# Kernel tuning notes

Measured on AMD Instinct MI355X. Metric: run time of the kernel, lower is better.

Reference implementation:

```python
import jax, jax.numpy as jnp
import numpy as np

N_NODES = 50000
N_EDGES = 800000
IN_F, HID, NCLS = 128, 64, 64
N_EXTRA = 2          # layer - 2
K_STEPS = 10
ALPHA = 0.1
BN_EPS = 1e-5


def setup_inputs() -> dict:
    key = jax.random.key(0)
    ks = jax.random.split(key, 20)
    d = {}
    d['x'] = jax.random.normal(ks[0], (N_NODES, IN_F), dtype=jnp.float32)
    d['edge_index'] = jax.random.randint(ks[1], (2, N_EDGES), 0, N_NODES, dtype=jnp.int64)
    s = 1.0 / np.sqrt(HID)
    d['W1'] = jax.random.normal(ks[2], (IN_F, HID), dtype=jnp.float32) / np.sqrt(IN_F)
    d['b1'] = jnp.zeros((HID,), jnp.float32)
    d['W2'] = jax.random.normal(ks[3], (HID, HID), dtype=jnp.float32) * s
    d['b2'] = jnp.zeros((HID,), jnp.float32)
    d['Wx'] = jax.random.normal(ks[4], (N_EXTRA, HID, HID), dtype=jnp.float32) * s
    d['bx'] = jnp.zeros((N_EXTRA, HID), jnp.float32)
    d['g1'] = jnp.ones((HID,), jnp.float32); d['be1'] = jnp.zeros((HID,), jnp.float32)
    d['g2'] = jnp.ones((HID,), jnp.float32); d['be2'] = jnp.zeros((HID,), jnp.float32)
    d['g3'] = jnp.ones((HID,), jnp.float32); d['be3'] = jnp.zeros((HID,), jnp.float32)
    d['Wfc'] = jax.random.normal(ks[5], (HID, NCLS), dtype=jnp.float32) * s
    d['bfc'] = jnp.zeros((NCLS,), jnp.float32)
    return d


def _gcn_norm(edge_index, n):
    # add self-loops, symmetric D^-1/2 (A+I) D^-1/2 normalization (PyG GCNConv default)
    loop = jnp.arange(n, dtype=edge_index.dtype)
    src = jnp.concatenate([edge_index[0], loop])
    dst = jnp.concatenate([edge_index[1], loop])
    deg = jax.ops.segment_sum(jnp.ones(src.shape[0], jnp.float32), dst, num_segments=n)
    dinv = jnp.where(deg > 0, jax.lax.rsqrt(deg), 0.0)
    return src, dst, dinv[src] * dinv[dst]


def _propagate(x, src, dst, w, n):
    # gather-scale-scatter: out[dst] += w * x[src]
    return jax.ops.segment_sum(x[src] * w[:, None], dst, num_segments=n)


def _bn(x, g, b):
    # BatchNorm1d in training mode: batch statistics over the node dim
    m = jnp.mean(x, axis=0)
    v = jnp.var(x, axis=0)
    return g * (x - m) * jax.lax.rsqrt(v + BN_EPS) + b


def reference(x, edge_index, W1, b1, W2, b2, Wx, bx, g1, be1, g2, be2, g3, be3, Wfc, bfc):
    n = x.shape[0]
    src, dst, w = _gcn_norm(edge_index, n)
    h = _propagate(x @ W1, src, dst, w, n) + b1
    h = jax.nn.relu(_bn(h, g1, be1))
    h = _propagate(h @ W2, src, dst, w, n) + b2
    h = jax.nn.relu(_bn(h, g2, be2))
    for i in range(Wx.shape[0]):
        h = _propagate(h @ Wx[i], src, dst, w, n) + bx[i]
        h = jax.nn.relu(_bn(h, g3, be3))
    # APPNP: K power-iteration steps with teleport back to h0
    h0 = h
    for _ in range(K_STEPS):
        h = (1.0 - ALPHA) * _propagate(h, src, dst, w, n) + ALPHA * h0
    out = h @ Wfc + bfc
    return jax.nn.log_softmax(out, axis=1)
```

## Files before the change

kernel.cpp:

```cpp
#include <hip/hip_runtime.h>
#include <hip/hip_fp16.h>
#include <cstdint>
#include <cstddef>

#define NN 50000
#define NE 800000
#define HID 64
#define INF_ 128
#define BN_EPS 1e-5f
#define NGRP (NN / 8)
#define NG16 (NN / 16)
#define SCAN_B 196
#define NSLICE 32
#define NBKT 16
#define NBIN 196
#define EPB 2048
#define BCAP 5120

typedef float floatx2 __attribute__((ext_vector_type(2)));

__device__ __forceinline__ float4 h8_to_f4(float2 raw) {
    union { float f; __half2 h; } ua, ub;
    ua.f = raw.x; ub.f = raw.y;
    float2 fa = __half22float2(ua.h), fb = __half22float2(ub.h);
    return make_float4(fa.x, fa.y, fb.x, fb.y);
}
__device__ __forceinline__ float2 f4_to_h8(float4 v) {
    union { float f; __half2 h; } ua, ub;
    ua.h = __float22half2_rn(make_float2(v.x, v.y));
    ub.h = __float22half2_rn(make_float2(v.z, v.w));
    return make_float2(ua.f, ub.f);
}
struct f8 { float v[8]; };
__device__ __forceinline__ f8 h16_to_f8(float4 raw) {
    f8 r;
    union { float f; __half2 h; } u;
    float2 a;
    u.f = raw.x; a = __half22float2(u.h); r.v[0] = a.x; r.v[1] = a.y;
    u.f = raw.y; a = __half22float2(u.h); r.v[2] = a.x; r.v[3] = a.y;
    u.f = raw.z; a = __half22float2(u.h); r.v[4] = a.x; r.v[5] = a.y;
    u.f = raw.w; a = __half22float2(u.h); r.v[6] = a.x; r.v[7] = a.y;
    return r;
}
__device__ __forceinline__ float4 f8_to_h16(const f8& s) {
    union { float f; __half2 h; } u;
    float4 o;
    u.h = __float22half2_rn(make_float2(s.v[0], s.v[1])); o.x = u.f;
    u.h = __float22half2_rn(make_float2(s.v[2], s.v[3])); o.y = u.f;
    u.h = __float22half2_rn(make_float2(s.v[4], s.v[5])); o.z = u.f;
    u.h = __float22half2_rn(make_float2(s.v[6], s.v[7])); o.w = u.f;
    return o;
}

__device__ __forceinline__ void fp8x8_to_f(unsigned lo, unsigned hi, float out[8]) {
    floatx2 a = __builtin_amdgcn_cvt_pk_f32_fp8((int)lo, false);
    floatx2 b = __builtin_amdgcn_cvt_pk_f32_fp8((int)lo, true);
    floatx2 c = __builtin_amdgcn_cvt_pk_f32_fp8((int)hi, false);
    floatx2 d = __builtin_amdgcn_cvt_pk_f32_fp8((int)hi, true);
    out[0] = a[0]; out[1] = a[1]; out[2] = b[0]; out[3] = b[1];
    out[4] = c[0]; out[5] = c[1]; out[6] = d[0]; out[7] = d[1];
}
__device__ __forceinline__ void fp8x16_to_f(uint4 r, float out[16]) {
    fp8x8_to_f(r.x, r.y, out);
    fp8x8_to_f(r.z, r.w, out + 8);
}
__device__ __forceinline__ uint2 f_to_fp8x8(const float v[8]) {
    int w0 = __builtin_amdgcn_cvt_pk_fp8_f32(v[0], v[1], 0, false);
    w0 = __builtin_amdgcn_cvt_pk_fp8_f32(v[2], v[3], w0, true);
    int w1 = __builtin_amdgcn_cvt_pk_fp8_f32(v[4], v[5], 0, false);
    w1 = __builtin_amdgcn_cvt_pk_fp8_f32(v[6], v[7], w1, true);
    uint2 o; o.x = (unsigned)w0; o.y = (unsigned)w1;
    return o;
}
__device__ __forceinline__ uint4 f_to_fp8x16(const float v[16]) {
    uint2 a = f_to_fp8x8(v), b = f_to_fp8x8(v + 8);
    uint4 o; o.x = a.x; o.y = a.y; o.z = b.x; o.w = b.y;
    return o;
}


__global__ __launch_bounds__(256) void binscat_k(
        const int* __restrict__ src, const int* __restrict__ dst,
        int* __restrict__ bcur, int2* __restrict__ pairs) {
    __shared__ int lcnt[256], lscan[256], lexc[256], gbase[256];
    __shared__ int2 stage[EPB];
    const int t = threadIdx.x;
    const int base = blockIdx.x * EPB;
    lcnt[t] = 0;
    __syncthreads();
    int2 mypair[EPB / 256];
    int mybin[EPB / 256], myr[EPB / 256];
#pragma unroll
    for (int i = 0; i < EPB / 256; ++i) {
        int e = base + i * 256 + t;
        if (e < NE) {
            int s = src[e], d = dst[e];
            mypair[i] = make_int2(s, d);
            mybin[i] = d >> 8;
            myr[i] = atomicAdd(&lcnt[mybin[i]], 1);
        } else mybin[i] = -1;
    }
    __syncthreads();
    lscan[t] = lcnt[t];
    __syncthreads();
    for (int d = 1; d < 256; d <<= 1) {
        int u = (t >= d) ? lscan[t - d] : 0;
        __syncthreads();
        lscan[t] += u;
        __syncthreads();
    }
    lexc[t] = lscan[t] - lcnt[t];
    if (lcnt[t] > 0) gbase[t] = atomicAdd(&bcur[t], lcnt[t]);
    __syncthreads();
#pragma unroll
    for (int i = 0; i < EPB / 256; ++i)
        if (mybin[i] >= 0) stage[lexc[mybin[i]] + myr[i]] = mypair[i];
    __syncthreads();
    const int total = lscan[255];
#pragma unroll
    for (int i = 0; i < EPB / 256; ++i) {
        int s = i * 256 + t;
        if (s < total) {
            int2 pr = stage[s];
            int b = pr.y >> 8;
            pairs[(size_t)b * BCAP + gbase[b] + (s - lexc[b])] = pr;
        }
    }
}

__global__ __launch_bounds__(256) void bincnt_k(
        const int2* __restrict__ pairs, const int* __restrict__ bcur,
        int* __restrict__ deg, float* __restrict__ dinv, int* __restrict__ hist) {
    __shared__ int lc[256];
    __shared__ int lh[NBKT];
    const int b = blockIdx.x, t = threadIdx.x;
    lc[t] = 0;
    if (t < NBKT) lh[t] = 0;
    __syncthreads();
    const int cnt = bcur[b];
    const size_t s0 = (size_t)b * BCAP;
    for (int s = t; s < cnt; s += 256)
        atomicAdd(&lc[pairs[s0 + s].y & 255], 1);
    __syncthreads();
    int n = b * 256 + t;
    if (n < NN) {
        int d = lc[t];
        deg[n] = d;
        dinv[n] = rsqrtf((float)(d + 1));
        int c = (d + 7) >> 3;
        if (c > NBKT - 1) c = NBKT - 1;
        atomicAdd(&lh[c], 1);
    }
    __syncthreads();
    if (t < NBKT && lh[t]) atomicAdd(&hist[t], lh[t]);
}

__global__ __launch_bounds__(256) void scan1perm_k(
        const int* __restrict__ deg, const int* __restrict__ hist,
        int* __restrict__ offs, int* __restrict__ bsum,
        int* __restrict__ bktcur, int* __restrict__ perm) {
    __shared__ int sh[256];
    __shared__ int lh[NBKT], lbase[NBKT];
    const int t = threadIdx.x, b = blockIdx.x;
    const int i = b * 256 + t;
    const int dg = (i < NN) ? deg[i] : 0;
    if (t < NBKT) lh[t] = 0;
    __syncthreads();
    int c = 0, r = 0;
    if (i < NN) {
        c = (dg + 7) >> 3;
        if (c > NBKT - 1) c = NBKT - 1;
        r = atomicAdd(&lh[c], 1);
    }
    __syncthreads();
    if (t < NBKT) {
        int s = 0;
        for (int k = 0; k < t; ++k) s += hist[k];
        lbase[t] = s + (lh[t] ? atomicAdd(&bktcur[t], lh[t]) : 0);
    }
    __syncthreads();
    if (i < NN) perm[lbase[c] + r] = i;
    int v = (i < NN) ? ((dg + 7) & ~7) : 0;
    sh[t] = v;
    __syncthreads();
    for (int d = 1; d < 256; d <<= 1) {
        int u = (t >= d) ? sh[t - d] : 0;
        __syncthreads();
        sh[t] += u;
        __syncthreads();
    }
    if (i < NN) offs[i] = sh[t] - v;
    if (t == 255) bsum[b] = sh[255];
}

__global__ __launch_bounds__(256) void scan23_k(
        const int* __restrict__ bsum, int* __restrict__ offs) {
    __shared__ int sh[256];
    const int t = threadIdx.x, b = blockIdx.x;
    int v = (t < SCAN_B) ? bsum[t] : 0;
    sh[t] = v;
    __syncthreads();
    for (int d = 1; d < 256; d <<= 1) {
        int u = (t >= d) ? sh[t - d] : 0;
        __syncthreads();
        sh[t] += u;
        __syncthreads();
    }
    const int bpre = (b > 0) ? sh[b - 1] : 0;
    const int total = sh[SCAN_B - 1];
    const int i = b * 256 + t;
    if (i < NN) offs[i] += bpre;
    if (i == NN) offs[NN] = total;
}

__global__ __launch_bounds__(256) void binplace_pad_k(
        const int* __restrict__ bcur, const int2* __restrict__ pairs,
        const int* __restrict__ offs, int* __restrict__ edge1,
        float4* __restrict__ tmpH, uint4* __restrict__ x8a,
        uint4* __restrict__ x8b) {
    __shared__ int lcur[256];
    const int b = blockIdx.x, t = threadIdx.x;
    if (b == 0) {
        if (t < 8) tmpH[(size_t)NN * 8 + t] = make_float4(0.f, 0.f, 0.f, 0.f);
        else if (t < 12) x8a[(size_t)NN * 4 + (t - 8)] = make_uint4(0, 0, 0, 0);
        else if (t < 16) x8b[(size_t)NN * 4 + (t - 12)] = make_uint4(0, 0, 0, 0);
    }
    lcur[t] = 0;
    __syncthreads();
    const int cnt = bcur[b];
    const size_t s0 = (size_t)b * BCAP;
    for (int s = t; s < cnt; s += 256) {
        int2 pr = pairs[s0 + s];
        int d = pr.y;
        int slot = atomicAdd(&lcur[d & 255], 1);
        edge1[offs[d] + slot] = pr.x;
    }
    __syncthreads();
    int n = b * 256 + t;
    if (n < NN) {
        int e = offs[n] + lcur[t], e1 = offs[n + 1];
        for (; e < e1; ++e) edge1[e] = NN;
    }
}

template <int K, bool HIN>
__global__ __launch_bounds__(256, 2) void mm_k(const void* __restrict__ Xv,
                                               const float* __restrict__ W,
                                               const float* __restrict__ dinv,
                                               float2* __restrict__ Y) {
    constexpr int RS = K + 4;
    __shared__ float Xs[64 * RS];
    __shared__ float Ws[K * 64];
    const int t = threadIdx.x;
    const int n0 = blockIdx.x * 64;

    {
        const float4* Wg = (const float4*)W;
        for (int g2 = t; g2 < K * 16; g2 += 256) {
            int row = g2 >> 4, c4 = g2 & 15;
            *(float4*)&Ws[row * 64 + c4 * 4] = Wg[g2];
        }
    }
    if (HIN) {
        const float4* Xg = (const float4*)Xv;
        for (int g2 = t; g2 < 64 * (K / 8); g2 += 256) {
            int row = g2 / (K / 8), c8 = g2 % (K / 8);
            int rr = n0 + row; if (rr >= NN) rr = NN - 1;
            f8 v = h16_to_f8(Xg[(size_t)rr * (K / 8) + c8]);
            float* dp = &Xs[row * RS + c8 * 8];
#pragma unroll
            for (int j = 0; j < 8; ++j) dp[j] = v.v[j];
        }
    } else {
        const float4* Xg = (const float4*)Xv;
        for (int g2 = t; g2 < 64 * (K / 4); g2 += 256) {
            int row = g2 / (K / 4), c4 = g2 % (K / 4);
            int rr = n0 + row; if (rr >= NN) rr = NN - 1;
            *(float4*)&Xs[row * RS + c4 * 4] = Xg[(size_t)rr * (K / 4) + c4];
        }
    }
    __syncthreads();

    const int r0 = (t >> 4) << 2;
    const int c0 = (t & 15) << 2;
    float acc[4][4];
#pragma unroll
    for (int j = 0; j < 4; ++j)
#pragma unroll
        for (int c = 0; c < 4; ++c) acc[j][c] = 0.f;

#pragma unroll 8
    for (int kq = 0; kq < K / 4; ++kq) {
        float4 xv[4];
#pragma unroll
        for (int j = 0; j < 4; ++j)
            xv[j] = *(const float4*)&Xs[(r0 + j) * RS + kq * 4];
        float4 wv[4];
#pragma unroll
        for (int i = 0; i < 4; ++i)
            wv[i] = *(const float4*)&Ws[(kq * 4 + i) * 64 + c0];
#pragma unroll
        for (int j = 0; j < 4; ++j) {
            acc[j][0] = fmaf(xv[j].x, wv[0].x, acc[j][0]);
            acc[j][1] = fmaf(xv[j].x, wv[0].y, acc[j][1]);
            acc[j][2] = fmaf(xv[j].x, wv[0].z, acc[j][2]);
            acc[j][3] = fmaf(xv[j].x, wv[0].w, acc[j][3]);
            acc[j][0] = fmaf(xv[j].y, wv[1].x, acc[j][0]);
            acc[j][1] = fmaf(xv[j].y, wv[1].y, acc[j][1]);
            acc[j][2] = fmaf(xv[j].y, wv[1].z, acc[j][2]);
            acc[j][3] = fmaf(xv[j].y, wv[1].w, acc[j][3]);
            acc[j][0] = fmaf(xv[j].z, wv[2].x, acc[j][0]);
            acc[j][1] = fmaf(xv[j].z, wv[2].y, acc[j][1]);
            acc[j][2] = fmaf(xv[j].z, wv[2].z, acc[j][2]);
            acc[j][3] = fmaf(xv[j].z, wv[2].w, acc[j][3]);
            acc[j][0] = fmaf(xv[j].w, wv[3].x, acc[j][0]);
            acc[j][1] = fmaf(xv[j].w, wv[3].y, acc[j][1]);
            acc[j][2] = fmaf(xv[j].w, wv[3].z, acc[j][2]);
            acc[j][3] = fmaf(xv[j].w, wv[3].w, acc[j][3]);
        }
    }

#pragma unroll
    for (int j = 0; j < 4; ++j) {
        int rr = n0 + r0 + j;
        if (rr < NN) {
            float dn = dinv[rr];
            Y[(size_t)rr * 16 + (t & 15)] =
                f4_to_h8(make_float4(acc[j][0] * dn, acc[j][1] * dn,
                                     acc[j][2] * dn, acc[j][3] * dn));
        }
    }
}

__global__ __launch_bounds__(256, 2) void mm_bn_k(
        const float4* __restrict__ Y4in, const float* __restrict__ slices,
        const float* __restrict__ gg, const float* __restrict__ be,
        const float* __restrict__ W, const float* __restrict__ dinv,
        float2* __restrict__ Y) {
    constexpr int K = 64, RS = K + 4;
    __shared__ float Xs[64 * RS];
    __shared__ float Ws[K * 64];
    __shared__ float fs[128], gs[64], bs[64];
    const int t = threadIdx.x;
    const int n0 = blockIdx.x * 64;

    if (t < 128) {
        float s = 0.f;
#pragma unroll
        for (int k = 0; k < NSLICE; ++k) s += slices[k * 128 + t];
        fs[t] = s;
    } else if (t < 192) {
        gs[t - 128] = gg[t - 128];
    } else {
        bs[t - 192] = be[t - 192];
    }
    {
        const float4* Wg = (const float4*)W;
        for (int g2 = t; g2 < K * 16; g2 += 256) {
            int row = g2 >> 4, c4 = g2 & 15;
            *(float4*)&Ws[row * 64 + c4 * 4] = Wg[g2];
        }
    }
    __syncthreads();

    const float invN = 1.f / (float)NN;
    for (int g2 = t; g2 < 64 * 8; g2 += 256) {
        int row = g2 >> 3, c8 = g2 & 7;
        int rr = n0 + row; if (rr >= NN) rr = NN - 1;
        f8 v = h16_to_f8(Y4in[(size_t)rr * 8 + c8]);
        float* dp = &Xs[row * RS + c8 * 8];
#pragma unroll
        for (int j = 0; j < 8; ++j) {
            int f = c8 * 8 + j;
            float m = fs[f] * invN;
            float va = fs[64 + f] * invN - m * m;
            float val = fmaf(gs[f] * rsqrtf(va + BN_EPS), v.v[j] - m, bs[f]);
            dp[j] = val > 0.f ? val : 0.f;
        }
    }
    __syncthreads();

    const int r0 = (t >> 4) << 2;
    const int c0 = (t & 15) << 2;
    float acc[4][4];
#pragma unroll
    for (int j = 0; j < 4; ++j)
#pragma unroll
        for (int c = 0; c < 4; ++c) acc[j][c] = 0.f;

#pragma unroll 8
    for (int kq = 0; kq < K / 4; ++kq) {
        float4 xv[4];
#pragma unroll
        for (int j = 0; j < 4; ++j)
            xv[j] = *(const float4*)&Xs[(r0 + j) * RS + kq * 4];
        float4 wv[4];
#pragma unroll
        for (int i = 0; i < 4; ++i)
            wv[i] = *(const float4*)&Ws[(kq * 4 + i) * 64 + c0];
#pragma unroll
        for (int j = 0; j < 4; ++j) {
            acc[j][0] = fmaf(xv[j].x, wv[0].x, acc[j][0]);
            acc[j][1] = fmaf(xv[j].x, wv[0].y, acc[j][1]);
            acc[j][2] = fmaf(xv[j].x, wv[0].z, acc[j][2]);
            acc[j][3] = fmaf(xv[j].x, wv[0].w, acc[j][3]);
            acc[j][0] = fmaf(xv[j].y, wv[1].x, acc[j][0]);
            acc[j][1] = fmaf(xv[j].y, wv[1].y, acc[j][1]);
            acc[j][2] = fmaf(xv[j].y, wv[1].z, acc[j][2]);
            acc[j][3] = fmaf(xv[j].y, wv[1].w, acc[j][3]);
            acc[j][0] = fmaf(xv[j].z, wv[2].x, acc[j][0]);
            acc[j][1] = fmaf(xv[j].z, wv[2].y, acc[j][1]);
            acc[j][2] = fmaf(xv[j].z, wv[2].z, acc[j][2]);
            acc[j][3] = fmaf(xv[j].z, wv[2].w, acc[j][3]);
            acc[j][0] = fmaf(xv[j].w, wv[3].x, acc[j][0]);
            acc[j][1] = fmaf(xv[j].w, wv[3].y, acc[j][1]);
            acc[j][2] = fmaf(xv[j].w, wv[3].z, acc[j][2]);
            acc[j][3] = fmaf(xv[j].w, wv[3].w, acc[j][3]);
        }
    }

#pragma unroll
    for (int j = 0; j < 4; ++j) {
        int rr = n0 + r0 + j;
        if (rr < NN) {
            float dn = dinv[rr];
            Y[(size_t)rr * 16 + (t & 15)] =
                f4_to_h8(make_float4(acc[j][0] * dn, acc[j][1] * dn,
                                     acc[j][2] * dn, acc[j][3] * dn));
        }
    }
}

__device__ __forceinline__ void prop_gather8(const float4* __restrict__ X4,
                                             const int* __restrict__ E,
                                             int e0, int e1, int fl, int slotbase,
                                             float acc[8]) {
    if (e0 >= e1) return;
    int d = E[e0 + fl];
    float4 ra[4];
#pragma unroll
    for (int i = 0; i < 4; ++i) {
        int s = __shfl(d, slotbase + i, 64);
        ra[i] = X4[(size_t)s * 8 + fl];
    }
    for (int e = e0; e < e1; e += 8) {
        float4 rb[4];
#pragma unroll
        for (int i = 0; i < 4; ++i) {
            int s = __shfl(d, slotbase + 4 + i, 64);
            rb[i] = X4[(size_t)s * 8 + fl];
        }
        bool more = (e + 8 < e1);
        if (more) d = E[e + 8 + fl];
        __builtin_amdgcn_sched_barrier(0);
#pragma unroll
        for (int i = 0; i < 4; ++i) {
            f8 x = h16_to_f8(ra[i]);
#pragma unroll
            for (int j = 0; j < 8; ++j) acc[j] += x.v[j];
        }
        if (more) {
#pragma unroll
            for (int i = 0; i < 4; ++i) {
                int s = __shfl(d, slotbase + i, 64);
                ra[i] = X4[(size_t)s * 8 + fl];
            }
        }
        __builtin_amdgcn_sched_barrier(0);
#pragma unroll
        for (int i = 0; i < 4; ++i) {
            f8 x = h16_to_f8(rb[i]);
#pragma unroll
            for (int j = 0; j < 8; ++j) acc[j] += x.v[j];
        }
    }
}

__global__ __launch_bounds__(256, 3) void prop_stats_k(
        const float4* __restrict__ X4, const int* __restrict__ offs,
        const int* __restrict__ edge1, const float* __restrict__ dinv,
        const float* __restrict__ bias, const int* __restrict__ perm,
        float4* __restrict__ Y4, float* __restrict__ stats) {
    const int lane = threadIdx.x & 63;
    const int wave = threadIdx.x >> 6;
    const int slot = lane >> 3;
    const int fl = lane & 7;
    const int slotbase = lane & 56;
    const int wid = blockIdx.x * 4 + wave;
    const int nw = gridDim.x * 4;

    float bias8[8];
    {
        float4 b0 = ((const float4*)bias)[fl * 2];
        float4 b1 = ((const float4*)bias)[fl * 2 + 1];
        bias8[0] = b0.x; bias8[1] = b0.y; bias8[2] = b0.z; bias8[3] = b0.w;
        bias8[4] = b1.x; bias8[5] = b1.y; bias8[6] = b1.z; bias8[7] = b1.w;
    }

    float s1[8], s2[8];
#pragma unroll
    for (int j = 0; j < 8; ++j) { s1[j] = 0.f; s2[j] = 0.f; }

    for (int g = wid; g < NGRP; g += nw) {
        int n = perm[g * 8 + slot];
        float dn = dinv[n];
        f8 self = h16_to_f8(X4[(size_t)n * 8 + fl]);
        float acc[8];
#pragma unroll
        for (int j = 0; j < 8; ++j) acc[j] = self.v[j];
        int e0 = offs[n], e1 = offs[n + 1];
        prop_gather8(X4, edge1, e0, e1, fl, slotbase, acc);
        f8 o;
#pragma unroll
        for (int j = 0; j < 8; ++j) {
            float a = fmaf(dn, acc[j], bias8[j]);
            o.v[j] = a;
            s1[j] += a;
            s2[j] = fmaf(a, a, s2[j]);
        }
        Y4[(size_t)n * 8 + fl] = f8_to_h16(o);
    }

#pragma unroll
    for (int m = 8; m <= 32; m <<= 1) {
#pragma unroll
        for (int j = 0; j < 8; ++j) {
            s1[j] += __shfl_xor(s1[j], m, 64);
            s2[j] += __shfl_xor(s2[j], m, 64);
        }
    }

    __shared__ float red[4][8][16];
    if (lane < 8) {
#pragma unroll
        for (int j = 0; j < 8; ++j) {
            red[wave][lane][j] = s1[j];
            red[wave][lane][8 + j] = s2[j];
        }
    }
    __syncthreads();
    int t = threadIdx.x;
    if (t < 128) {
        int j = t & 63;
        int isq = t >> 6;
        int fli = j >> 3, c = (j & 7) + isq * 8;
        float a = red[0][fli][c] + red[1][fli][c] + red[2][fli][c] + red[3][fli][c];
        atomicAdd(&stats[(blockIdx.x & (NSLICE - 1)) * 128 + isq * 64 + j], a);
    }
}

__global__ __launch_bounds__(256) void bn_relu_k(
        const float4* __restrict__ Y4, const float* __restrict__ slices,
        const float* __restrict__ g, const float* __restrict__ be,
        float4* __restrict__ H4, uint2* __restrict__ X8,
        const float* __restrict__ dinv) {
    __shared__ float fs[128];
    int t = threadIdx.x;
    if (t < 128) {
        float s = 0.f;
#pragma unroll
        for (int k = 0; k < NSLICE; ++k) s += slices[k * 128 + t];
        fs[t] = s;
    }
    __syncthreads();
    int i = blockIdx.x * blockDim.x + t;
    if (i >= NN * 8) return;
    int fg = i & 7;
    const float invN = 1.f / (float)NN;
    f8 y = h16_to_f8(Y4[i]);
    float4 gv0 = ((const float4*)g)[fg * 2];
    float4 gv1 = ((const float4*)g)[fg * 2 + 1];
    float4 bv0 = ((const float4*)be)[fg * 2];
    float4 bv1 = ((const float4*)be)[fg * 2 + 1];
    float gv[8] = { gv0.x, gv0.y, gv0.z, gv0.w, gv1.x, gv1.y, gv1.z, gv1.w };
    float bv[8] = { bv0.x, bv0.y, bv0.z, bv0.w, bv1.x, bv1.y, bv1.z, bv1.w };
    f8 o;
#pragma unroll
    for (int j = 0; j < 8; ++j) {
        float m = fs[fg * 8 + j] * invN;
        float v = fs[64 + fg * 8 + j] * invN - m * m;
        float val = fmaf(gv[j] * rsqrtf(v + BN_EPS), y.v[j] - m, bv[j]);
        o.v[j] = val > 0.f ? val : 0.f;
    }
    H4[i] = f8_to_h16(o);
    {
        float dn = dinv[i >> 3];
        float sv[8];
#pragma unroll
        for (int j = 0; j < 8; ++j) sv[j] = dn * o.v[j];
        X8[i] = f_to_fp8x8(sv);
    }
}

template <bool OUT16>
__global__ __launch_bounds__(256, 3) void appnp8_k(
        const uint4* __restrict__ X8, const float4* __restrict__ H04,
        const int* __restrict__ offs, const int* __restrict__ edge1,
        const float* __restrict__ dinv, const int* __restrict__ perm,
        uint4* __restrict__ Y8, float4* __restrict__ Y16) {
    const int lane = threadIdx.x & 63;
    const int wave = threadIdx.x >> 6;
    const int slot = lane >> 2;
    const int fl = lane & 3;
    const int quadbase = lane & 60;
    const int wid = blockIdx.x * 4 + wave;
    if (wid >= NG16) return;
    int n = perm[wid * 16 + slot];
    float dn = dinv[n];
    float acc[16];
    {
        float self[16];
        fp8x16_to_f(X8[(size_t)n * 4 + fl], self);
#pragma unroll
        for (int j = 0; j < 16; ++j) acc[j] = self[j];
    }
    int e0 = offs[n], e1 = offs[n + 1];
    if (e0 < e1) {
        int2 d = ((const int2*)(edge1 + e0))[fl];
        uint4 ra[4];
#pragma unroll
        for (int k = 0; k < 4; ++k) {
            int s = __shfl((k & 1) ? d.y : d.x, quadbase + (k >> 1), 64);
            ra[k] = X8[(size_t)s * 4 + fl];
        }
        for (int e = e0; e < e1; e += 8) {
            uint4 rb[4];
#pragma unroll
            for (int k = 0; k < 4; ++k) {
                int s = __shfl((k & 1) ? d.y : d.x, quadbase + 2 + (k >> 1), 64);
                rb[k] = X8[(size_t)s * 4 + fl];
            }
            bool more = (e + 8 < e1);
            if (more) d = ((const int2*)(edge1 + e + 8))[fl];
            __builtin_amdgcn_sched_barrier(0);
#pragma unroll
            for (int k = 0; k < 4; ++k) {
                float x[16];
                fp8x16_to_f(ra[k], x);
#pragma unroll
                for (int j = 0; j < 16; ++j) acc[j] += x[j];
            }
            if (more) {
#pragma unroll
                for (int k = 0; k < 4; ++k) {
                    int s = __shfl((k & 1) ? d.y : d.x, quadbase + (k >> 1), 64);
                    ra[k] = X8[(size_t)s * 4 + fl];
                }
            }
            __builtin_amdgcn_sched_barrier(0);
#pragma unroll
            for (int k = 0; k < 4; ++k) {
                float x[16];
                fp8x16_to_f(rb[k], x);
#pragma unroll
                for (int j = 0; j < 16; ++j) acc[j] += x[j];
            }
        }
    }
    f8 ha = h16_to_f8(H04[(size_t)n * 8 + fl * 2]);
    f8 hb = h16_to_f8(H04[(size_t)n * 8 + fl * 2 + 1]);
    float o[16];
    float s = 0.9f * dn;
#pragma unroll
    for (int j = 0; j < 8; ++j) {
        o[j] = fmaf(s, acc[j], 0.1f * ha.v[j]);
        o[8 + j] = fmaf(s, acc[8 + j], 0.1f * hb.v[j]);
    }
    if (OUT16) {
        f8 lo, hi;
#pragma unroll
        for (int j = 0; j < 8; ++j) { lo.v[j] = o[j]; hi.v[j] = o[8 + j]; }
        Y16[(size_t)n * 8 + fl * 2] = f8_to_h16(lo);
        Y16[(size_t)n * 8 + fl * 2 + 1] = f8_to_h16(hi);
    } else {
        float so[16];
#pragma unroll
        for (int j = 0; j < 16; ++j) so[j] = dn * o[j];
        Y8[(size_t)n * 4 + fl] = f_to_fp8x16(so);
    }
}

__global__ __launch_bounds__(256) void final_k(const float2* __restrict__ H2,
                                               const float* __restrict__ Wfc,
                                               const float* __restrict__ bfc,
                                               float* __restrict__ out) {
    const int t = threadIdx.x;
    const int n0 = blockIdx.x * 64;
    const int r0 = (t >> 4) << 2;
    const int c0 = (t & 15) << 2;

    int r[4];
#pragma unroll
    for (int j = 0; j < 4; ++j) {
        int rr = n0 + r0 + j;
        r[j] = rr < NN ? rr : NN - 1;
    }
    const float2* Xr[4];
#pragma unroll
    for (int j = 0; j < 4; ++j) Xr[j] = H2 + (size_t)r[j] * 16;

    float4 bf = *(const float4*)(bfc + c0);
    float acc[4][4];
#pragma unroll
    for (int j = 0; j < 4; ++j) {
        acc[j][0] = bf.x; acc[j][1] = bf.y; acc[j][2] = bf.z; acc[j][3] = bf.w;
    }

#pragma unroll 4
    for (int kq = 0; kq < 16; ++kq) {
        float4 xv[4];
#pragma unroll
        for (int j = 0; j < 4; ++j) xv[j] = h8_to_f4(Xr[j][kq]);
        float4 wv[4];
#pragma unroll
        for (int i = 0; i < 4; ++i)
            wv[i] = *(const float4*)(Wfc + (size_t)(kq * 4 + i) * 64 + c0);
#pragma unroll
        for (int j = 0; j < 4; ++j) {
            acc[j][0] = fmaf(xv[j].x, wv[0].x, acc[j][0]);
            acc[j][1] = fmaf(xv[j].x, wv[0].y, acc[j][1]);
            acc[j][2] = fmaf(xv[j].x, wv[0].z, acc[j][2]);
            acc[j][3] = fmaf(xv[j].x, wv[0].w, acc[j][3]);
            acc[j][0] = fmaf(xv[j].y, wv[1].x, acc[j][0]);
            acc[j][1] = fmaf(xv[j].y, wv[1].y, acc[j][1]);
            acc[j][2] = fmaf(xv[j].y, wv[1].z, acc[j][2]);
            acc[j][3] = fmaf(xv[j].y, wv[1].w, acc[j][3]);
            acc[j][0] = fmaf(xv[j].z, wv[2].x, acc[j][0]);
            acc[j][1] = fmaf(xv[j].z, wv[2].y, acc[j][1]);
            acc[j][2] = fmaf(xv[j].z, wv[2].z, acc[j][2]);
            acc[j][3] = fmaf(xv[j].z, wv[2].w, acc[j][3]);
            acc[j][0] = fmaf(xv[j].w, wv[3].x, acc[j][0]);
            acc[j][1] = fmaf(xv[j].w, wv[3].y, acc[j][1]);
            acc[j][2] = fmaf(xv[j].w, wv[3].z, acc[j][2]);
            acc[j][3] = fmaf(xv[j].w, wv[3].w, acc[j][3]);
        }
    }

#pragma unroll
    for (int j = 0; j < 4; ++j) {
        float m = fmaxf(fmaxf(acc[j][0], acc[j][1]), fmaxf(acc[j][2], acc[j][3]));
#pragma unroll
        for (int d = 1; d <= 8; d <<= 1) m = fmaxf(m, __shfl_xor(m, d, 64));
        float s = expf(acc[j][0] - m) + expf(acc[j][1] - m) +
                  expf(acc[j][2] - m) + expf(acc[j][3] - m);
#pragma unroll
        for (int d = 1; d <= 8; d <<= 1) s += __shfl_xor(s, d, 64);
        float lse = m + logf(s);
        int rr = n0 + r0 + j;
        if (rr < NN)
            *(float4*)(out + (size_t)rr * 64 + c0) =
                make_float4(acc[j][0] - lse, acc[j][1] - lse,
                            acc[j][2] - lse, acc[j][3] - lse);
    }
}


static inline char* alignup(char* p, size_t a) {
    return (char*)(((uintptr_t)p + a - 1) & ~(uintptr_t)(a - 1));
}

extern "C" void kernel_launch(void* const* d_in, const int* in_sizes, int n_in,
                              void* d_out, int out_size, void* d_ws, size_t ws_size,
                              hipStream_t stream) {
    const float* x   = (const float*)d_in[0];
    const int*   ei  = (const int*)d_in[1];
    const float* W1  = (const float*)d_in[2];
    const float* b1  = (const float*)d_in[3];
    const float* W2  = (const float*)d_in[4];
    const float* b2  = (const float*)d_in[5];
    const float* Wx  = (const float*)d_in[6];
    const float* bx  = (const float*)d_in[7];
    const float* g1  = (const float*)d_in[8];
    const float* be1 = (const float*)d_in[9];
    const float* g2  = (const float*)d_in[10];
    const float* be2 = (const float*)d_in[11];
    const float* g3  = (const float*)d_in[12];
    const float* be3 = (const float*)d_in[13];
    const float* Wfc = (const float*)d_in[14];
    const float* bfc = (const float*)d_in[15];
    float* out = (float*)d_out;

    const int* srcA = ei;
    const int* dstA = ei + NE;

    char* p = (char*)d_ws;
    float* stats  = (float*)p; p += 4 * NSLICE * 128 * 4;
    int*   hist   = (int*)p;   p += NBKT * 4;
    int*   bbcur  = (int*)p;   p += 256 * 4;
    int*   bktcur = (int*)p;   p += NBKT * 4;
    size_t zbytes = (size_t)(p - (char*)d_ws);
    p = alignup(p, 512);
    int*   deg   = (int*)p;    p += NN * 4;         p = alignup(p, 512);
    int*   offs  = (int*)p;    p += (NN + 4) * 4;   p = alignup(p, 512);
    float* dinv  = (float*)p;  p += NN * 4;         p = alignup(p, 512);
    int*   bsum  = (int*)p;    p += 256 * 4;        p = alignup(p, 512);
    int*   perm  = (int*)p;    p += NN * 4;         p = alignup(p, 512);
    int*   edge1 = (int*)p;    p += ((size_t)NE + 8 * NN + 256) * 4; p = alignup(p, 512);
    int2*  pairs = (int2*)p;   p += (size_t)NBIN * BCAP * 8; p = alignup(p, 512);
    float4* tmpH = (float4*)p; p += ((size_t)NN + 1) * 128; p = alignup(p, 512);
    float4* hbH  = (float4*)p; p += (size_t)NN * 128;       p = alignup(p, 512);
    float4* apH  = (float4*)p; p += (size_t)NN * 128;       p = alignup(p, 512);
    float4* pbH  = (float4*)p; p += (size_t)NN * 128;       p = alignup(p, 512);
    uint4*  x8a  = (uint4*)p;  p += ((size_t)NN + 1) * 64;  p = alignup(p, 512);
    uint4*  x8b  = (uint4*)p;  p += ((size_t)NN + 1) * 64;

    hipMemsetAsync(d_ws, 0, zbytes, stream);

    binscat_k<<<(NE + EPB - 1) / EPB, 256, 0, stream>>>(srcA, dstA, bbcur, pairs);
    bincnt_k<<<NBIN, 256, 0, stream>>>(pairs, bbcur, deg, dinv, hist);
    scan1perm_k<<<SCAN_B, 256, 0, stream>>>(deg, hist, offs, bsum, bktcur, perm);
    scan23_k<<<SCAN_B, 256, 0, stream>>>(bsum, offs);
    binplace_pad_k<<<NBIN, 256, 0, stream>>>(bbcur, pairs, offs, edge1, tmpH, x8a, x8b);

    const int MMG = (NN + 63) / 64;
    const int PG  = (NGRP + 3) / 4;
    const int AG  = (NG16 + 3) / 4;
    const int BNG = (NN * 8 + 255) / 256;
    const int SL  = NSLICE * 128;

    mm_k<INF_, false><<<MMG, 256, 0, stream>>>(x, W1, dinv, (float2*)tmpH);
    prop_stats_k<<<PG, 256, 0, stream>>>(tmpH, offs, edge1, dinv, b1, perm, pbH, stats + 0 * SL);
    mm_bn_k<<<MMG, 256, 0, stream>>>(pbH, stats + 0 * SL, g1, be1, W2, dinv, (float2*)tmpH);
    prop_stats_k<<<PG, 256, 0, stream>>>(tmpH, offs, edge1, dinv, b2, perm, pbH, stats + 1 * SL);
    mm_bn_k<<<MMG, 256, 0, stream>>>(pbH, stats + 1 * SL, g2, be2, Wx, dinv, (float2*)tmpH);
    prop_stats_k<<<PG, 256, 0, stream>>>(tmpH, offs, edge1, dinv, bx, perm, pbH, stats + 2 * SL);
    mm_bn_k<<<MMG, 256, 0, stream>>>(pbH, stats + 2 * SL, g3, be3,
                                     Wx + (size_t)64 * 64, dinv, (float2*)tmpH);
    prop_stats_k<<<PG, 256, 0, stream>>>(tmpH, offs, edge1, dinv, bx + 64, perm,
                                         pbH, stats + 3 * SL);
    bn_relu_k<<<BNG, 256, 0, stream>>>(pbH, stats + 3 * SL, g3, be3, hbH, (uint2*)x8a, dinv);

    const uint4* cur8 = x8a;
    for (int it = 0; it < 9; ++it) {
        uint4* o8 = (cur8 == x8a) ? x8b : x8a;
        appnp8_k<false><<<AG, 256, 0, stream>>>(cur8, hbH, offs, edge1, dinv, perm, o8, nullptr);
        cur8 = o8;
    }
    appnp8_k<true><<<AG, 256, 0, stream>>>(cur8, hbH, offs, edge1, dinv, perm, nullptr, apH);

    final_k<<<MMG, 256, 0, stream>>>((const float2*)apH, Wfc, bfc, out);
}
```

Measured before the change: 425.4 us.

## Fuse final APPNP step with FC+log_softmax and merge offset scan into binplace

The last APPNP propagation step now computes the FC layer and log_softmax in-register and writes the output directly. This removes the fp16 intermediate buffer and the separate final kernel launch. Separately, the second-level scan is folded into binplace_pad_k: each block rescans the block sums and its local degrees, so the scan23 launch goes away and the local offsets stay in shared memory. In exchange the final kernel reads Wfc redundantly per lane with many shuffles, and every binplace block repeats the small block-sum scan.

New measurement: 510.7 us. +20.0%, slower.

```diff
diff --git a/kernel.cpp b/kernel.cpp
--- a/kernel.cpp
+++ b/kernel.cpp
@@ -157,8 +157,8 @@
 
 __global__ __launch_bounds__(256) void scan1perm_k(
         const int* __restrict__ deg, const int* __restrict__ hist,
-        int* __restrict__ offs, int* __restrict__ bsum,
-        int* __restrict__ bktcur, int* __restrict__ perm) {
+        int* __restrict__ bsum, int* __restrict__ bktcur,
+        int* __restrict__ perm) {
     __shared__ int sh[256];
     __shared__ int lh[NBKT], lbase[NBKT];
     const int t = threadIdx.x, b = blockIdx.x;
@@ -183,41 +183,21 @@
     int v = (i < NN) ? ((dg + 7) & ~7) : 0;
     sh[t] = v;
     __syncthreads();
-    for (int d = 1; d < 256; d <<= 1) {
-        int u = (t >= d) ? sh[t - d] : 0;
+    for (int d = 128; d > 0; d >>= 1) {
+        if (t < d) sh[t] += sh[t + d];
         __syncthreads();
-        sh[t] += u;
-        __syncthreads();
-    }
-    if (i < NN) offs[i] = sh[t] - v;
-    if (t == 255) bsum[b] = sh[255];
-}
-
-__global__ __launch_bounds__(256) void scan23_k(
-        const int* __restrict__ bsum, int* __restrict__ offs) {
-    __shared__ int sh[256];
-    const int t = threadIdx.x, b = blockIdx.x;
-    int v = (t < SCAN_B) ? bsum[t] : 0;
-    sh[t] = v;
-    __syncthreads();
-    for (int d = 1; d < 256; d <<= 1) {
-        int u = (t >= d) ? sh[t - d] : 0;
-        __syncthreads();
-        sh[t] += u;
-        __syncthreads();
-    }
-    const int bpre = (b > 0) ? sh[b - 1] : 0;
-    const int total = sh[SCAN_B - 1];
-    const int i = b * 256 + t;
-    if (i < NN) offs[i] += bpre;
-    if (i == NN) offs[NN] = total;
+    }
+    if (t == 0) bsum[b] = sh[0];
 }
 
 __global__ __launch_bounds__(256) void binplace_pad_k(
+        const int* __restrict__ deg, const int* __restrict__ bsum,
         const int* __restrict__ bcur, const int2* __restrict__ pairs,
-        const int* __restrict__ offs, int* __restrict__ edge1,
+        int* __restrict__ offs, int* __restrict__ edge1,
         float4* __restrict__ tmpH, uint4* __restrict__ x8a,
         uint4* __restrict__ x8b) {
+    __shared__ int sh[256];
+    __shared__ int loff[257];
     __shared__ int lcur[256];
     const int b = blockIdx.x, t = threadIdx.x;
     if (b == 0) {
@@ -225,20 +205,47 @@
         else if (t < 12) x8a[(size_t)NN * 4 + (t - 8)] = make_uint4(0, 0, 0, 0);
         else if (t < 16) x8b[(size_t)NN * 4 + (t - 12)] = make_uint4(0, 0, 0, 0);
     }
+    int v = (t < SCAN_B) ? bsum[t] : 0;
+    sh[t] = v;
+    __syncthreads();
+    for (int d = 1; d < 256; d <<= 1) {
+        int u = (t >= d) ? sh[t - d] : 0;
+        __syncthreads();
+        sh[t] += u;
+        __syncthreads();
+    }
+    const int bpre = (b > 0) ? sh[b - 1] : 0;
+    const int total = sh[SCAN_B - 1];
+    __syncthreads();
+    const int n = b * 256 + t;
+    const int dg = (n < NN) ? deg[n] : 0;
+    const int pv = (n < NN) ? ((dg + 7) & ~7) : 0;
+    sh[t] = pv;
+    __syncthreads();
+    for (int d = 1; d < 256; d <<= 1) {
+        int u = (t >= d) ? sh[t - d] : 0;
+        __syncthreads();
+        sh[t] += u;
+        __syncthreads();
+    }
+    const int myoff = bpre + sh[t] - pv;
+    loff[t] = myoff;
+    if (t == 255) loff[256] = bpre + sh[255];
+    if (n < NN) offs[n] = myoff;
+    if (n == NN) offs[NN] = total;
     lcur[t] = 0;
     __syncthreads();
     const int cnt = bcur[b];
     const size_t s0 = (size_t)b * BCAP;
     for (int s = t; s < cnt; s += 256) {
         int2 pr = pairs[s0 + s];
-        int d = pr.y;
-        int slot = atomicAdd(&lcur[d & 255], 1);
-        edge1[offs[d] + slot] = pr.x;
-    }
-    __syncthreads();
-    int n = b * 256 + t;
+        int d = pr.y & 255;
+        int slot = atomicAdd(&lcur[d], 1);
+        edge1[loff[d] + slot] = pr.x;
+    }
+    __syncthreads();
     if (n < NN) {
-        int e = offs[n] + lcur[t], e1 = offs[n + 1];
+        int e = loff[t] + lcur[t], e1 = loff[t + 1];
         for (; e < e1; ++e) edge1[e] = NN;
     }
 }
@@ -592,12 +599,65 @@
     }
 }
 
-template <bool OUT16>
+__device__ __forceinline__ void appnp_gather(
+        const uint4* __restrict__ X8, const int* __restrict__ offs,
+        const int* __restrict__ edge1, int n, int fl, int quadbase,
+        float acc[16]) {
+    {
+        float self[16];
+        fp8x16_to_f(X8[(size_t)n * 4 + fl], self);
+#pragma unroll
+        for (int j = 0; j < 16; ++j) acc[j] = self[j];
+    }
+    int e0 = offs[n], e1 = offs[n + 1];
+    if (e0 >= e1) return;
+    int2 d = ((const int2*)(edge1 + e0))[fl];
+    uint4 ra[4];
+#pragma unroll
+    for (int k = 0; k < 4; ++k) {
+        int s = __shfl((k & 1) ? d.y : d.x, quadbase + (k >> 1), 64);
+        ra[k] = X8[(size_t)s * 4 + fl];
+    }
+    for (int e = e0; e < e1; e += 8) {
+        uint4 rb[4];
+#pragma unroll
+        for (int k = 0; k < 4; ++k) {
+            int s = __shfl((k & 1) ? d.y : d.x, quadbase + 2 + (k >> 1), 64);
+            rb[k] = X8[(size_t)s * 4 + fl];
+        }
+        bool more = (e + 8 < e1);
+        if (more) d = ((const int2*)(edge1 + e + 8))[fl];
+        __builtin_amdgcn_sched_barrier(0);
+#pragma unroll
+        for (int k = 0; k < 4; ++k) {
+            float x[16];
+            fp8x16_to_f(ra[k], x);
+#pragma unroll
+            for (int j = 0; j < 16; ++j) acc[j] += x[j];
+        }
+        if (more) {
+#pragma unroll
+            for (int k = 0; k < 4; ++k) {
+                int s = __shfl((k & 1) ? d.y : d.x, quadbase + (k >> 1), 64);
+                ra[k] = X8[(size_t)s * 4 + fl];
+            }
+        }
+        __builtin_amdgcn_sched_barrier(0);
+#pragma unroll
+        for (int k = 0; k < 4; ++k) {
+            float x[16];
+            fp8x16_to_f(rb[k], x);
+#pragma unroll
+            for (int j = 0; j < 16; ++j) acc[j] += x[j];
+        }
+    }
+}
+
 __global__ __launch_bounds__(256, 3) void appnp8_k(
         const uint4* __restrict__ X8, const float4* __restrict__ H04,
         const int* __restrict__ offs, const int* __restrict__ edge1,
         const float* __restrict__ dinv, const int* __restrict__ perm,
-        uint4* __restrict__ Y8, float4* __restrict__ Y16) {
+        uint4* __restrict__ Y8) {
     const int lane = threadIdx.x & 63;
     const int wave = threadIdx.x >> 6;
     const int slot = lane >> 2;
@@ -608,55 +668,7 @@
     int n = perm[wid * 16 + slot];
     float dn = dinv[n];
     float acc[16];
-    {
-        float self[16];
-        fp8x16_to_f(X8[(size_t)n * 4 + fl], self);
-#pragma unroll
-        for (int j = 0; j < 16; ++j) acc[j] = self[j];
-    }
-    int e0 = offs[n], e1 = offs[n + 1];
-    if (e0 < e1) {
-        int2 d = ((const int2*)(edge1 + e0))[fl];
-        uint4 ra[4];
-#pragma unroll
-        for (int k = 0; k < 4; ++k) {
-            int s = __shfl((k & 1) ? d.y : d.x, quadbase + (k >> 1), 64);
-            ra[k] = X8[(size_t)s * 4 + fl];
-        }
-        for (int e = e0; e < e1; e += 8) {
-            uint4 rb[4];
-#pragma unroll
-            for (int k = 0; k < 4; ++k) {
-                int s = __shfl((k & 1) ? d.y : d.x, quadbase + 2 + (k >> 1), 64);
-                rb[k] = X8[(size_t)s * 4 + fl];
-            }
-            bool more = (e + 8 < e1);
-            if (more) d = ((const int2*)(edge1 + e + 8))[fl];
-            __builtin_amdgcn_sched_barrier(0);
-#pragma unroll
-            for (int k = 0; k < 4; ++k) {
-                float x[16];
-                fp8x16_to_f(ra[k], x);
-#pragma unroll
-                for (int j = 0; j < 16; ++j) acc[j] += x[j];
-            }
-            if (more) {
-#pragma unroll
-                for (int k = 0; k < 4; ++k) {
-                    int s = __shfl((k & 1) ? d.y : d.x, quadbase + (k >> 1), 64);
-                    ra[k] = X8[(size_t)s * 4 + fl];
-                }
-            }
-            __builtin_amdgcn_sched_barrier(0);
-#pragma unroll
-            for (int k = 0; k < 4; ++k) {
-                float x[16];
-                fp8x16_to_f(rb[k], x);
-#pragma unroll
-                for (int j = 0; j < 16; ++j) acc[j] += x[j];
-            }
-        }
-    }
+    appnp_gather(X8, offs, edge1, n, fl, quadbase, acc);
     f8 ha = h16_to_f8(H04[(size_t)n * 8 + fl * 2]);
     f8 hb = h16_to_f8(H04[(size_t)n * 8 + fl * 2 + 1]);
     float o[16];
@@ -666,92 +678,81 @@
         o[j] = fmaf(s, acc[j], 0.1f * ha.v[j]);
         o[8 + j] = fmaf(s, acc[8 + j], 0.1f * hb.v[j]);
     }
-    if (OUT16) {
-        f8 lo, hi;
-#pragma unroll
-        for (int j = 0; j < 8; ++j) { lo.v[j] = o[j]; hi.v[j] = o[8 + j]; }
-        Y16[(size_t)n * 8 + fl * 2] = f8_to_h16(lo);
-        Y16[(size_t)n * 8 + fl * 2 + 1] = f8_to_h16(hi);
-    } else {
-        float so[16];
-#pragma unroll
-        for (int j = 0; j < 16; ++j) so[j] = dn * o[j];
-        Y8[(size_t)n * 4 + fl] = f_to_fp8x16(so);
-    }
-}
-
-__global__ __launch_bounds__(256) void final_k(const float2* __restrict__ H2,
-                                               const float* __restrict__ Wfc,
-                                               const float* __restrict__ bfc,
-                                               float* __restrict__ out) {
-    const int t = threadIdx.x;
-    const int n0 = blockIdx.x * 64;
-    const int r0 = (t >> 4) << 2;
-    const int c0 = (t & 15) << 2;
-
-    int r[4];
-#pragma unroll
-    for (int j = 0; j < 4; ++j) {
-        int rr = n0 + r0 + j;
-        r[j] = rr < NN ? rr : NN - 1;
-    }
-    const float2* Xr[4];
-#pragma unroll
-    for (int j = 0; j < 4; ++j) Xr[j] = H2 + (size_t)r[j] * 16;
-
-    float4 bf = *(const float4*)(bfc + c0);
-    float acc[4][4];
-#pragma unroll
-    for (int j = 0; j < 4; ++j) {
-        acc[j][0] = bf.x; acc[j][1] = bf.y; acc[j][2] = bf.z; acc[j][3] = bf.w;
-    }
-
-#pragma unroll 4
-    for (int kq = 0; kq < 16; ++kq) {
-        float4 xv[4];
-#pragma unroll
-        for (int j = 0; j < 4; ++j) xv[j] = h8_to_f4(Xr[j][kq]);
-        float4 wv[4];
-#pragma unroll
-        for (int i = 0; i < 4; ++i)
-            wv[i] = *(const float4*)(Wfc + (size_t)(kq * 4 + i) * 64 + c0);
-#pragma unroll
-        for (int j = 0; j < 4; ++j) {
-            acc[j][0] = fmaf(xv[j].x, wv[0].x, acc[j][0]);
-            acc[j][1] = fmaf(xv[j].x, wv[0].y, acc[j][1]);
-            acc[j][2] = fmaf(xv[j].x, wv[0].z, acc[j][2]);
-            acc[j][3] = fmaf(xv[j].x, wv[0].w, acc[j][3]);
-            acc[j][0] = fmaf(xv[j].y, wv[1].x, acc[j][0]);
-            acc[j][1] = fmaf(xv[j].y, wv[1].y, acc[j][1]);
-            acc[j][2] = fmaf(xv[j].y, wv[1].z, acc[j][2]);
-            acc[j][3] = fmaf(xv[j].y, wv[1].w, acc[j][3]);
-            acc[j][0] = fmaf(xv[j].z, wv[2].x, acc[j][0]);
-            acc[j][1] = fmaf(xv[j].z, wv[2].y, acc[j][1]);
-            acc[j][2] = fmaf(xv[j].z, wv[2].z, acc[j][2]);
-            acc[j][3] = fmaf(xv[j].z, wv[2].w, acc[j][3]);
-            acc[j][0] = fmaf(xv[j].w, wv[3].x, acc[j][0]);
-            acc[j][1] = fmaf(xv[j].w, wv[3].y, acc[j][1]);
-            acc[j][2] = fmaf(xv[j].w, wv[3].z, acc[j][2]);
-            acc[j][3] = fmaf(xv[j].w, wv[3].w, acc[j][3]);
-        }
-    }
-
-#pragma unroll
-    for (int j = 0; j < 4; ++j) {
-        float m = fmaxf(fmaxf(acc[j][0], acc[j][1]), fmaxf(acc[j][2], acc[j][3]));
-#pragma unroll
-        for (int d = 1; d <= 8; d <<= 1) m = fmaxf(m, __shfl_xor(m, d, 64));
-        float s = expf(acc[j][0] - m) + expf(acc[j][1] - m) +
-                  expf(acc[j][2] - m) + expf(acc[j][3] - m);
-#pragma unroll
-        for (int d = 1; d <= 8; d <<= 1) s += __shfl_xor(s, d, 64);
-        float lse = m + logf(s);
-        int rr = n0 + r0 + j;
-        if (rr < NN)
-            *(float4*)(out + (size_t)rr * 64 + c0) =
-                make_float4(acc[j][0] - lse, acc[j][1] - lse,
-                            acc[j][2] - lse, acc[j][3] - lse);
-    }
+    float so[16];
+#pragma unroll
+    for (int j = 0; j < 16; ++j) so[j] = dn * o[j];
+    Y8[(size_t)n * 4 + fl] = f_to_fp8x16(so);
+}
+
+__global__ __launch_bounds__(256, 2) void appnp_final_k(
+        const uint4* __restrict__ X8, const float4* __restrict__ H04,
+        const int* __restrict__ offs, const int* __restrict__ edge1,
+        const float* __restrict__ dinv, const int* __restrict__ perm,
+        const float* __restrict__ Wfc, const float* __restrict__ bfc,
+        float* __restrict__ out) {
+    const int lane = threadIdx.x & 63;
+    const int wave = threadIdx.x >> 6;
+    const int slot = lane >> 2;
+    const int fl = lane & 3;
+    const int quadbase = lane & 60;
+    const int wid = blockIdx.x * 4 + wave;
+    if (wid >= NG16) return;
+    int n = perm[wid * 16 + slot];
+    float dn = dinv[n];
+    float acc[16];
+    appnp_gather(X8, offs, edge1, n, fl, quadbase, acc);
+    f8 ha = h16_to_f8(H04[(size_t)n * 8 + fl * 2]);
+    f8 hb = h16_to_f8(H04[(size_t)n * 8 + fl * 2 + 1]);
+    float h[16];
+    float s9 = 0.9f * dn;
+#pragma unroll
+    for (int j = 0; j < 8; ++j) {
+        h[j] = fmaf(s9, acc[j], 0.1f * ha.v[j]);
+        h[8 + j] = fmaf(s9, acc[8 + j], 0.1f * hb.v[j]);
+    }
+    float fc[16];
+    {
+        const float4* bp = (const float4*)(bfc + fl * 16);
+#pragma unroll
+        for (int q = 0; q < 4; ++q) {
+            float4 bq = bp[q];
+            fc[q * 4 + 0] = bq.x; fc[q * 4 + 1] = bq.y;
+            fc[q * 4 + 2] = bq.z; fc[q * 4 + 3] = bq.w;
+        }
+    }
+#pragma unroll
+    for (int q = 0; q < 4; ++q) {
+#pragma unroll
+        for (int j = 0; j < 16; ++j) {
+            float hk = __shfl(h[j], quadbase + q, 64);
+            const float4* wr = (const float4*)(Wfc + (size_t)(q * 16 + j) * 64 + fl * 16);
+            float4 w0 = wr[0], w1 = wr[1], w2 = wr[2], w3 = wr[3];
+            fc[0]  = fmaf(hk, w0.x, fc[0]);  fc[1]  = fmaf(hk, w0.y, fc[1]);
+            fc[2]  = fmaf(hk, w0.z, fc[2]);  fc[3]  = fmaf(hk, w0.w, fc[3]);
+            fc[4]  = fmaf(hk, w1.x, fc[4]);  fc[5]  = fmaf(hk, w1.y, fc[5]);
+            fc[6]  = fmaf(hk, w1.z, fc[6]);  fc[7]  = fmaf(hk, w1.w, fc[7]);
+            fc[8]  = fmaf(hk, w2.x, fc[8]);  fc[9]  = fmaf(hk, w2.y, fc[9]);
+            fc[10] = fmaf(hk, w2.z, fc[10]); fc[11] = fmaf(hk, w2.w, fc[11]);
+            fc[12] = fmaf(hk, w3.x, fc[12]); fc[13] = fmaf(hk, w3.y, fc[13]);
+            fc[14] = fmaf(hk, w3.z, fc[14]); fc[15] = fmaf(hk, w3.w, fc[15]);
+        }
+    }
+    float m = fc[0];
+#pragma unroll
+    for (int j = 1; j < 16; ++j) m = fmaxf(m, fc[j]);
+    m = fmaxf(m, __shfl_xor(m, 1, 64));
+    m = fmaxf(m, __shfl_xor(m, 2, 64));
+    float s = 0.f;
+#pragma unroll
+    for (int j = 0; j < 16; ++j) s += expf(fc[j] - m);
+    s += __shfl_xor(s, 1, 64);
+    s += __shfl_xor(s, 2, 64);
+    float lse = m + logf(s);
+    float* op = out + (size_t)n * 64 + fl * 16;
+#pragma unroll
+    for (int q = 0; q < 4; ++q)
+        *(float4*)(op + q * 4) = make_float4(fc[q * 4 + 0] - lse, fc[q * 4 + 1] - lse,
+                                             fc[q * 4 + 2] - lse, fc[q * 4 + 3] - lse);
 }
 
 
@@ -799,7 +800,6 @@
     int2*  pairs = (int2*)p;   p += (size_t)NBIN * BCAP * 8; p = alignup(p, 512);
     float4* tmpH = (float4*)p; p += ((size_t)NN + 1) * 128; p = alignup(p, 512);
     float4* hbH  = (float4*)p; p += (size_t)NN * 128;       p = alignup(p, 512);
-    float4* apH  = (float4*)p; p += (size_t)NN * 128;       p = alignup(p, 512);
     float4* pbH  = (float4*)p; p += (size_t)NN * 128;       p = alignup(p, 512);
     uint4*  x8a  = (uint4*)p;  p += ((size_t)NN + 1) * 64;  p = alignup(p, 512);
     uint4*  x8b  = (uint4*)p;  p += ((size_t)NN + 1) * 64;
@@ -808,9 +808,9 @@
 
     binscat_k<<<(NE + EPB - 1) / EPB, 256, 0, stream>>>(srcA, dstA, bbcur, pairs);
     bincnt_k<<<NBIN, 256, 0, stream>>>(pairs, bbcur, deg, dinv, hist);
-    scan1perm_k<<<SCAN_B, 256, 0, stream>>>(deg, hist, offs, bsum, bktcur, perm);
-    scan23_k<<<SCAN_B, 256, 0, stream>>>(bsum, offs);
-    binplace_pad_k<<<NBIN, 256, 0, stream>>>(bbcur, pairs, offs, edge1, tmpH, x8a, x8b);
+    scan1perm_k<<<SCAN_B, 256, 0, stream>>>(deg, hist, bsum, bktcur, perm);
+    binplace_pad_k<<<NBIN, 256, 0, stream>>>(deg, bsum, bbcur, pairs, offs, edge1,
+                                             tmpH, x8a, x8b);
 
     const int MMG = (NN + 63) / 64;
     const int PG  = (NGRP + 3) / 4;
@@ -833,10 +833,9 @@
     const uint4* cur8 = x8a;
     for (int it = 0; it < 9; ++it) {
         uint4* o8 = (cur8 == x8a) ? x8b : x8a;
-        appnp8_k<false><<<AG, 256, 0, stream>>>(cur8, hbH, offs, edge1, dinv, perm, o8, nullptr);
+        appnp8_k<<<AG, 256, 0, stream>>>(cur8, hbH, offs, edge1, dinv, perm, o8);
         cur8 = o8;
     }
-    appnp8_k<true><<<AG, 256, 0, stream>>>(cur8, hbH, offs, edge1, dinv, perm, nullptr, apH);
-
-    final_k<<<MMG, 256, 0, stream>>>((const float2*)apH, Wfc, bfc, out);
-}
+    appnp_final_k<<<AG, 256, 0, stream>>>(cur8, hbH, offs, edge1, dinv, perm,
+                                          Wfc, bfc, out);
+}
```
